# Optimization experiments

Hardware: AMD Instinct MI355X
Metric: run time of the kernel (lower is better)

## Reference

```python
import jax, jax.numpy as jnp
import numpy as np

EPS = 1e-6
H = 8          # num_heads
GAMMA = 0.99   # fixed decay (requires_grad=False in source)
RPE_LAYERS = 3


def srms(x):
    # SimpleRMSNorm: x / (rms(x) + eps), rms = ||x||_2 / sqrt(d) = sqrt(mean(x^2))
    return x / (jnp.sqrt(jnp.mean(x * x, axis=-1, keepdims=True)) + EPS)


def setup_inputs() -> dict:
    key = jax.random.key(0)
    B, N, E = 8, 2048, 512
    D1 = 1536            # int(3*512) // 8 * 8
    R = 512              # rpe_embedding
    ks = jax.random.split(key, 12)

    def lin(k, i, o):
        return jax.random.normal(k, (i, o), jnp.float32) * (i ** -0.5)

    x = jax.random.normal(ks[0], (B, N, E), jnp.float32)
    return {
        "x": x,
        "Wu": lin(ks[1], E, D1), "bu": jnp.zeros((D1,), jnp.float32),
        "Wv": lin(ks[2], E, D1), "bv": jnp.zeros((D1,), jnp.float32),
        "Wo": lin(ks[3], D1, E), "bo": jnp.zeros((E,), jnp.float32),
        "rpe_Win": lin(ks[4], 1, R), "rpe_bin": jnp.zeros((R,), jnp.float32),
        "rpe_W": jax.random.normal(ks[5], (RPE_LAYERS, R, R), jnp.float32) * (R ** -0.5),
        "rpe_b": jnp.zeros((RPE_LAYERS, R), jnp.float32),
        "rpe_Wout": lin(ks[6], R, D1), "rpe_bout": jnp.zeros((D1,), jnp.float32),
    }


def reference(x, Wu, bu, Wv, bv, Wo, bo, rpe_Win, rpe_bin, rpe_W, rpe_b, rpe_Wout, rpe_bout):
    B, N, E = x.shape
    u = jax.nn.silu(x @ Wu + bu)                     # b n d1
    v = jax.nn.silu(x @ Wv + bv)                     # b n d1
    D1 = v.shape[-1]
    D = D1 // H
    v = v.reshape(B, N, H, D).transpose(0, 2, 1, 3)  # b h n d

    # RPE MLP over positions: row 0 is the zero index, rows 1..N-1 are pos indices 1..N-1 (par_type=1)
    idx = jnp.arange(0, N, dtype=x.dtype)[:, None]   # (N, 1)
    h = idx @ rpe_Win + rpe_bin                      # (N, R)
    for i in range(RPE_LAYERS):                      # residual=False
        h = jax.nn.relu(srms(h)) @ rpe_W[i] + rpe_b[i]
    coeffs = jax.nn.relu(srms(h)) @ rpe_Wout + rpe_bout   # (N, H*D)
    coeffs = coeffs.reshape(N, H, D).transpose(1, 0, 2)   # h n d

    zero = coeffs[:, :1]                             # h 1 d  (a_0)
    pos = coeffs[:, 1:]                              # h n-1 d (a_1..a_{n-1})
    decay = GAMMA ** jnp.arange(1, N, dtype=x.dtype)[None, :, None]
    pos = pos * decay
    # causal: a = [a0, a1..a_{n-1}, a0]; act_type='none' -> identity
    a = jnp.concatenate([zero, pos, zero], axis=1)   # h, n+1, d

    # Toeplitz mixing via circular convolution of length 2n (torch.fft.rfft/irfft, norm='backward')
    m = 2 * N
    yf = jnp.fft.rfft(v, m, axis=2)                  # b h m/2+1 d (complex)
    af = jnp.fft.rfft(a, m, axis=1)[None]            # 1 h m/2+1 d
    out = jnp.fft.irfft(yf * af, m, axis=2)[:, :, :N, :]  # b h n d

    out = out.transpose(0, 2, 1, 3).reshape(B, N, D1)     # b n (h d)
    out = u * out
    return out @ Wo + bo
```

## Files before the change

### kernel.cpp

```cpp
#include <hip/hip_runtime.h>
#include <cstdint>


typedef unsigned short ushort_t;
typedef __attribute__((ext_vector_type(8))) short short8;
typedef __attribute__((ext_vector_type(4))) float f32x4;

#define AS1 __attribute__((address_space(1)))
#define AS3 __attribute__((address_space(3)))

#define SWZ(j) ((j) ^ (((j) >> 4) & 14))

__device__ __forceinline__ float bf2f(ushort_t b) {
  union { unsigned u; float f; } x; x.u = ((unsigned)b) << 16; return x.f;
}
__device__ __forceinline__ ushort_t f2bf(float f) {
  union { float f; unsigned u; } x; x.f = f;
  unsigned r = x.u + 0x7fffu + ((x.u >> 16) & 1u);
  return (ushort_t)(r >> 16);
}

__device__ __forceinline__ void gload_lds16(const void* g, void* l) {
  auto gp = reinterpret_cast<const AS1 unsigned*>(reinterpret_cast<uintptr_t>(g));
  auto lp = reinterpret_cast<AS3 unsigned*>(reinterpret_cast<uintptr_t>(l));
  __builtin_amdgcn_global_load_lds(gp, lp, 16, 0, 0);
}

template<int MODE>
__launch_bounds__(256, 2)
__global__ void gemm_bt(const ushort_t* __restrict__ A, const ushort_t* __restrict__ Bt,
                        const float* __restrict__ bias, void* __restrict__ Cout,
                        void* __restrict__ Cout2, int M, int N, int K, float lng)
{
  __shared__ ushort_t As[128 * 64];
  __shared__ ushort_t Bs[128 * 64];
  const int tid  = threadIdx.x;
  const int wave = tid >> 6, lane = tid & 63;
  const int nb = N >> 7;
  const int bm = (int)blockIdx.x / nb, bn = (int)blockIdx.x % nb;
  const int m0 = bm << 7, n0 = bn << 7;
  const int lrow = lane & 15, quad = lane >> 4;
  const int wm = (wave >> 1) << 6, wn = (wave & 1) << 6;
  const int srow = lane >> 3;
  const int scol = (lane & 7) << 3;

  f32x4 acc[4][4] = {};

  for (int kt = 0; kt < K; kt += 64) {
    __syncthreads();
#pragma unroll
    for (int i = 0; i < 4; ++i) {
      const int ci  = i * 4 + wave;
      const int row = ci * 8 + srow;
      gload_lds16(A  + (long)(m0 + row) * K + kt + scol, (void*)&As[ci * 512]);
      gload_lds16(Bt + (long)(n0 + row) * K + kt + scol, (void*)&Bs[ci * 512]);
    }
    __syncthreads();
#pragma unroll
    for (int s = 0; s < 2; ++s) {
      short8 afr[4], bfr[4];
#pragma unroll
      for (int i = 0; i < 4; ++i)
        afr[i] = *(const short8*)&As[(wm + i * 16 + lrow) * 64 + s * 32 + quad * 8];
#pragma unroll
      for (int j = 0; j < 4; ++j)
        bfr[j] = *(const short8*)&Bs[(wn + j * 16 + lrow) * 64 + s * 32 + quad * 8];
#pragma unroll
      for (int i = 0; i < 4; ++i)
#pragma unroll
        for (int j = 0; j < 4; ++j)
          acc[i][j] = __builtin_amdgcn_mfma_f32_16x16x32_bf16(afr[i], bfr[j], acc[i][j], 0, 0, 0);
    }
  }

#pragma unroll
  for (int i = 0; i < 4; ++i) {
    const int rowb = m0 + wm + i * 16 + quad * 4;
#pragma unroll
    for (int j = 0; j < 4; ++j) {
      const int col = n0 + wn + j * 16 + lrow;
      const float bv = bias[col];
      if (MODE == 0) {
#pragma unroll
        for (int r = 0; r < 4; ++r)
          ((float*)Cout)[(long)(rowb + r) * N + col] = acc[i][j][r] + bv;
      } else if (MODE == 2) {
#pragma unroll
        for (int r = 0; r < 4; ++r) {
          const int row = rowb + r;
          float dec = __expf(lng * (float)row);
          ((float*)Cout)[(long)col * M + row] = (acc[i][j][r] + bv) * dec;
        }
      } else {
        if (col < 1536) {
#pragma unroll
          for (int r = 0; r < 4; ++r) {
            float val = acc[i][j][r] + bv;
            float sv = val / (1.f + __expf(-val));
            ((ushort_t*)Cout)[(long)(rowb + r) * 1536 + col] = f2bf(sv);
          }
        } else {
          union { ushort_t h[4]; uint2 u2; } pk;
#pragma unroll
          for (int r = 0; r < 4; ++r) {
            float val = acc[i][j][r] + bv;
            float sv = val / (1.f + __expf(-val));
            pk.h[r] = f2bf(sv);
          }
          *(uint2*)((ushort_t*)Cout2 + (long)(col - 1536) * 16384 + rowb) = pk.u2;
        }
      }
    }
  }
}

__device__ __forceinline__ void srms_relu_store(float v0, float v1, ushort_t* out,
                                                long rowbase, int tid)
{
  float ss = v0 * v0 + v1 * v1;
#pragma unroll
  for (int off = 32; off; off >>= 1) ss += __shfl_down(ss, off);
  __shared__ float ps[4];
  const int wave = tid >> 6, lane = tid & 63;
  if (lane == 0) ps[wave] = ss;
  __syncthreads();
  float tot = ps[0] + ps[1] + ps[2] + ps[3];
  float sc = 1.f / (sqrtf(tot * (1.f / 512.f)) + 1e-6f);
  out[rowbase + tid]       = f2bf(fmaxf(v0 * sc, 0.f));
  out[rowbase + tid + 256] = f2bf(fmaxf(v1 * sc, 0.f));
}

__launch_bounds__(256)
__global__ void rpe_norm(const float* __restrict__ h, ushort_t* __restrict__ out)
{
  const int n = blockIdx.x, tid = threadIdx.x;
  float v0 = h[(long)n * 512 + tid];
  float v1 = h[(long)n * 512 + tid + 256];
  srms_relu_store(v0, v1, out, (long)n * 512, tid);
}

__device__ __forceinline__ void wtrans_body(const float* __restrict__ src,
                                            ushort_t* __restrict__ dst,
                                            int K, int N, int lb, int tid,
                                            float (*tile)[33])
{
  const int nbx = N >> 5;
  const int bx = lb % nbx, by = lb / nbx;
  const int n0 = bx << 5, k0 = by << 5;
  const int tx = tid & 31, ty = tid >> 5;
  for (int yy = ty; yy < 32; yy += 8)
    tile[yy][tx] = src[(long)(k0 + yy) * N + n0 + tx];
  __syncthreads();
  for (int yy = ty; yy < 32; yy += 8)
    dst[(long)(n0 + yy) * K + k0 + tx] = f2bf(tile[tx][yy]);
}

__launch_bounds__(256)
__global__ void prep_all(const float* __restrict__ Wu, const float* __restrict__ Wv,
                         const float* __restrict__ Wo, const float* __restrict__ rW,
                         const float* __restrict__ rWout,
                         const float* __restrict__ bu, const float* __restrict__ bv,
                         const float* __restrict__ x,
                         const float* __restrict__ rWin, const float* __restrict__ rbin,
                         ushort_t* __restrict__ wuvt, ushort_t* __restrict__ wot,
                         ushort_t* __restrict__ wrt, ushort_t* __restrict__ wroutt,
                         float* __restrict__ buvb, ushort_t* __restrict__ xb,
                         float2* __restrict__ twg, float2* __restrict__ twh,
                         ushort_t* __restrict__ a0)
{
  __shared__ float tile[32][33];
  const int bid = blockIdx.x, tid = threadIdx.x;
  if (bid < 3840) {
    const float* src; ushort_t* dst; int K, N, lb;
    if (bid < 768)       { src = Wu;    dst = wuvt;              K = 512;  N = 1536; lb = bid; }
    else if (bid < 1536) { src = Wv;    dst = wuvt + 1536L*512;  K = 512;  N = 1536; lb = bid - 768; }
    else if (bid < 2304) { src = Wo;    dst = wot;               K = 1536; N = 512;  lb = bid - 1536; }
    else if (bid < 2560) { src = rW;              dst = wrt;              K = 512; N = 512; lb = bid - 2304; }
    else if (bid < 2816) { src = rW + 512L*512;   dst = wrt + 512L*512;   K = 512; N = 512; lb = bid - 2560; }
    else if (bid < 3072) { src = rW + 2L*512*512; dst = wrt + 2L*512*512; K = 512; N = 512; lb = bid - 2816; }
    else                 { src = rWout; dst = wroutt;            K = 512;  N = 1536; lb = bid - 3072; }
    wtrans_body(src, dst, K, N, lb, tid, tile);
  } else if (bid < 3846) {
    int i = (bid - 3840) * 256 + tid;
    if (i < 1536) { buvb[i] = bu[i]; buvb[1536 + i] = bv[i]; }
  } else if (bid < 12038) {
    long i = (long)(bid - 3846) * 1024 + tid * 4;
    float4 f = *(const float4*)(x + i);
    unsigned lo = (unsigned)f2bf(f.x) | ((unsigned)f2bf(f.y) << 16);
    unsigned hi = (unsigned)f2bf(f.z) | ((unsigned)f2bf(f.w) << 16);
    *(uint2*)(xb + i) = make_uint2(lo, hi);
  } else if (bid < 12046) {
    int j = (bid - 12038) * 256 + tid;
    float s, c;
    __sincosf((float)j * (6.283185307179586f / 2048.f), &s, &c);
    twg[j] = make_float2(c, -s);
    if (j <= 1024) {
      float s2, c2;
      __sincosf((float)j * (3.14159265358979f / 2048.f), &s2, &c2);
      twh[j] = make_float2(c2, -s2);
    }
  } else {
    const int n = bid - 12046;
    const float fn = (float)n;
    float v0 = fn * rWin[tid] + rbin[tid];
    float v1 = fn * rWin[tid + 256] + rbin[tid + 256];
    srms_relu_store(v0, v1, a0, (long)n * 512, tid);
  }
}

__device__ __forceinline__ float2 cmulf(float2 a, float2 b) {
  return make_float2(a.x * b.x - a.y * b.y, a.x * b.y + a.y * b.x);
}

__device__ void fft2048_lds(float2* bx, float2* by, const float2* __restrict__ tw, int tid)
{
#pragma unroll
  for (int ii = 0; ii < 4; ++ii) {
    const int i = tid + ii * 256;
    float2 a = bx[SWZ(i)], b = bx[SWZ(i + 1024)];
    const int s = SWZ(2 * i);
    by[s]     = make_float2(a.x + b.x, a.y + b.y);
    by[s + 1] = make_float2(a.x - b.x, a.y - b.y);
  }
  __syncthreads();
  float2* src = by; float2* dst = bx;
#pragma unroll
  for (int ps = 0; ps < 5; ++ps) {
    const int p = 2 << (2 * ps);
    const int ts = 512 / p;
#pragma unroll
    for (int ii = 0; ii < 2; ++ii) {
      const int i = tid + ii * 256;
      const int k = i & (p - 1);
      float2 u0 = src[SWZ(i)],        u1 = src[SWZ(i + 512)];
      float2 u2 = src[SWZ(i + 1024)], u3 = src[SWZ(i + 1536)];
      const int tb = k * ts;
      float2 w1 = tw[tb], w2 = tw[2 * tb], w3 = tw[3 * tb];
      u1 = cmulf(u1, w1); u2 = cmulf(u2, w2); u3 = cmulf(u3, w3);
      float2 v0 = make_float2(u0.x + u2.x, u0.y + u2.y);
      float2 v2 = make_float2(u0.x - u2.x, u0.y - u2.y);
      float2 v1 = make_float2(u1.x + u3.x, u1.y + u3.y);
      float2 v3 = make_float2(u1.y - u3.y, u3.x - u1.x);
      const int j = ((i - k) << 2) + k;
      dst[SWZ(j)]         = make_float2(v0.x + v1.x, v0.y + v1.y);
      dst[SWZ(j + p)]     = make_float2(v2.x + v3.x, v2.y + v3.y);
      dst[SWZ(j + 2*p)]   = make_float2(v0.x - v1.x, v0.y - v1.y);
      dst[SWZ(j + 3*p)]   = make_float2(v2.x - v3.x, v2.y - v3.y);
    }
    __syncthreads();
    float2* t = src; src = dst; dst = t;
  }
}

__launch_bounds__(256)
__global__ void fft_kernel_spec(const float* __restrict__ kern, float2* __restrict__ af,
                                const float2* __restrict__ twg, const float2* __restrict__ twh)
{
  __shared__ float2 bx[2048], by[2048];
  const int tid = threadIdx.x, c = blockIdx.x;
  const float* kc = kern + (long)c * 2048;
  for (int j = tid; j < 1024; j += 256) bx[SWZ(j)] = *(const float2*)(kc + 2 * j);
  for (int j = tid + 1024; j < 2048; j += 256) bx[SWZ(j)] = make_float2(0.f, 0.f);
  __syncthreads();
  fft2048_lds(bx, by, twg, tid);
  float2* afc = af + (long)c * 2052;
  for (int k = tid; k <= 1024; k += 256) {
    float2 Zk = bx[SWZ(k)], Zn = bx[SWZ((2048 - k) & 2047)];
    float2 E = make_float2(0.5f * (Zk.x + Zn.x), 0.5f * (Zk.y - Zn.y));
    float2 O = make_float2(0.5f * (Zk.y + Zn.y), 0.5f * (Zn.x - Zk.x));
    float2 W = twh[k];
    float2 WO = cmulf(W, O);
    afc[k] = make_float2(E.x + WO.x, E.y + WO.y);
    if (k != 0 && k != 1024)
      afc[2048 - k] = make_float2(E.x - WO.x, -(E.y - WO.y));
    if (k == 0)
      afc[2048] = make_float2(E.x - WO.x, -(E.y - WO.y));
  }
}

__launch_bounds__(256)
__global__ void fft_conv(ushort_t* __restrict__ vt, const float2* __restrict__ af,
                         const float2* __restrict__ twg, const float2* __restrict__ twh)
{
  __shared__ float2 bx[2048], by[2048];
  const int tid = threadIdx.x;
  const int c = (int)blockIdx.x >> 3;
  ushort_t* vs = vt + (long)blockIdx.x * 2048;
  for (int j = tid; j < 1024; j += 256) {
    unsigned pv = *(const unsigned*)(vs + 2 * j);
    bx[SWZ(j)] = make_float2(bf2f((ushort_t)(pv & 0xffffu)), bf2f((ushort_t)(pv >> 16)));
  }
  for (int j = tid + 1024; j < 2048; j += 256) bx[SWZ(j)] = make_float2(0.f, 0.f);
  __syncthreads();
  fft2048_lds(bx, by, twg, tid);
  const float2* afc = af + (long)c * 2052;
  for (int k = tid; k <= 1024; k += 256) {
    float2 Zk = bx[SWZ(k)], Zn = bx[SWZ((2048 - k) & 2047)];
    float2 E = make_float2(0.5f * (Zk.x + Zn.x), 0.5f * (Zk.y - Zn.y));
    float2 O = make_float2(0.5f * (Zk.y + Zn.y), 0.5f * (Zn.x - Zk.x));
    float2 W = twh[k];
    float2 WO = cmulf(W, O);
    float2 Xk = make_float2(E.x + WO.x, E.y + WO.y);
    float2 Xn = make_float2(E.x - WO.x, -(E.y - WO.y));
    float2 Pk = cmulf(Xk, afc[k]);
    float2 Pn = cmulf(Xn, afc[2048 - k]);
    float2 E2 = make_float2(0.5f * (Pk.x + Pn.x), 0.5f * (Pk.y - Pn.y));
    float2 G  = make_float2(0.5f * (Pk.x - Pn.x), 0.5f * (Pk.y + Pn.y));
    float2 cW = make_float2(W.x, -W.y);
    float2 Fo = cmulf(cW, G);
    by[SWZ(k)] = make_float2(E2.x - Fo.y, -(E2.y + Fo.x));
    if (k != 0 && k != 1024) {
      const int kn = 2048 - k;
      by[SWZ(kn)] = make_float2(E2.x + Fo.y, E2.y - Fo.x);
    }
  }
  __syncthreads();
  fft2048_lds(by, bx, twg, tid);
  const float inv = 1.f / 2048.f;
  for (int j = tid; j < 1024; j += 256) {
    float2 r = by[SWZ(j)];
    unsigned ov = (unsigned)f2bf(r.x * inv) | ((unsigned)f2bf(-r.y * inv) << 16);
    *(unsigned*)(vs + 2 * j) = ov;
  }
}

__launch_bounds__(256)
__global__ void gate_trans(const ushort_t* __restrict__ convt, ushort_t* __restrict__ u)
{
  __shared__ ushort_t tile[64][65];
  const int bc = (int)blockIdx.x % 24, br = (int)blockIdx.x / 24;
  const int c0 = bc << 6, r0 = br << 6;
  const int tx = threadIdx.x & 63, ty = threadIdx.x >> 6;
  for (int yy = ty; yy < 64; yy += 4)
    tile[yy][tx] = convt[(long)(c0 + yy) * 16384 + r0 + tx];
  __syncthreads();
  for (int yy = ty; yy < 64; yy += 4) {
    long ui = (long)(r0 + yy) * 1536 + c0 + tx;
    float uu = bf2f(u[ui]);
    float cc = bf2f(tile[tx][yy]);
    u[ui] = f2bf(uu * cc);
  }
}

extern "C" void kernel_launch(void* const* d_in, const int* in_sizes, int n_in,
                              void* d_out, int out_size, void* d_ws, size_t ws_size,
                              hipStream_t stream)
{
  const float* x     = (const float*)d_in[0];
  const float* Wu    = (const float*)d_in[1];
  const float* bu    = (const float*)d_in[2];
  const float* Wv    = (const float*)d_in[3];
  const float* bv    = (const float*)d_in[4];
  const float* Wo    = (const float*)d_in[5];
  const float* bo    = (const float*)d_in[6];
  const float* rWin  = (const float*)d_in[7];
  const float* rbin  = (const float*)d_in[8];
  const float* rW    = (const float*)d_in[9];
  const float* rb    = (const float*)d_in[10];
  const float* rWout = (const float*)d_in[11];
  const float* rbout = (const float*)d_in[12];

  char* base = (char*)d_ws;
  size_t off = 0;
  auto alloc = [&](size_t bytes) -> char* {
    size_t r = (off + 255) & ~(size_t)255; off = r + bytes; return base + r;
  };
  ushort_t* wuvt   = (ushort_t*)alloc(3072L * 512 * 2);
  ushort_t* wot    = (ushort_t*)alloc(512L * 1536 * 2);
  ushort_t* wrt    = (ushort_t*)alloc(3L * 512 * 512 * 2);
  ushort_t* wroutt = (ushort_t*)alloc(1536L * 512 * 2);
  float*    buvb   = (float*)   alloc(3072L * 4);
  ushort_t* a0     = (ushort_t*)alloc(2048L * 512 * 2);
  float2*   af     = (float2*)  alloc(1536L * 2052 * 8);
  float2*   twg    = (float2*)  alloc(2048L * 8);
  float2*   twh    = (float2*)  alloc(1025L * 8);
  char*     X      = alloc(16384L * 512 * 2);
  ushort_t* u      = (ushort_t*)alloc(16384L * 1536 * 2);
  ushort_t* vt     = (ushort_t*)alloc(1536L * 16384 * 2);
  ushort_t* xb   = (ushort_t*)X;
  float*    h    = (float*)X;
  float*    kern = (float*)(X + 4L * 1024 * 1024);

  const float lng = -0.01005033585350145f;

  prep_all<<<dim3(14094), dim3(256), 0, stream>>>(
      Wu, Wv, Wo, rW, rWout, bu, bv, x, rWin, rbin,
      wuvt, wot, wrt, wroutt, buvb, xb, twg, twh, a0);

  gemm_bt<3><<<dim3(3072), dim3(256), 0, stream>>>(xb, wuvt, buvb, u, vt,
                                                   16384, 3072, 512, 0.f);

  for (int i = 0; i < 3; ++i) {
    gemm_bt<0><<<dim3(64), dim3(256), 0, stream>>>(a0, wrt + (long)i * 512 * 512,
                                                   rb + (long)i * 512, h, nullptr,
                                                   2048, 512, 512, 0.f);
    rpe_norm<<<dim3(2048), dim3(256), 0, stream>>>(h, a0);
  }
  gemm_bt<2><<<dim3(192), dim3(256), 0, stream>>>(a0, wroutt, rbout, kern, nullptr,
                                                  2048, 1536, 512, lng);
  fft_kernel_spec<<<dim3(1536), dim3(256), 0, stream>>>(kern, af, twg, twh);

  fft_conv<<<dim3(12288), dim3(256), 0, stream>>>(vt, af, twg, twh);
  gate_trans<<<dim3(6144), dim3(256), 0, stream>>>(vt, u);
  gemm_bt<0><<<dim3(512), dim3(256), 0, stream>>>(u, wot, bo, d_out, nullptr,
                                                  16384, 512, 1536, 0.f);
}
```

Baseline: 530.8 us.

## Replace radix-2/4 LDS FFT with radix-8 stages and half-zero first pass

```diff
diff --git a/kernel.cpp b/kernel.cpp
--- a/kernel.cpp
+++ b/kernel.cpp
@@ -9,7 +9,8 @@
 #define AS1 __attribute__((address_space(1)))
 #define AS3 __attribute__((address_space(3)))
 
-#define SWZ(j) ((j) ^ (((j) >> 4) & 14))
+#define SW1(j) ((j) ^ (((j) >> 4) & 15))
+#define SW2(j) ((j) ^ ((((j) >> 6) & 7) << 1))
 
 __device__ __forceinline__ float bf2f(ushort_t b) {
   union { unsigned u; float f; } x; x.u = ((unsigned)b) << 16; return x.f;
@@ -211,45 +212,87 @@
 __device__ __forceinline__ float2 cmulf(float2 a, float2 b) {
   return make_float2(a.x * b.x - a.y * b.y, a.x * b.y + a.y * b.x);
 }
-
-__device__ void fft2048_lds(float2* bx, float2* by, const float2* __restrict__ tw, int tid)
-{
-#pragma unroll
-  for (int ii = 0; ii < 4; ++ii) {
-    const int i = tid + ii * 256;
-    float2 a = bx[SWZ(i)], b = bx[SWZ(i + 1024)];
-    const int s = SWZ(2 * i);
-    by[s]     = make_float2(a.x + b.x, a.y + b.y);
-    by[s + 1] = make_float2(a.x - b.x, a.y - b.y);
-  }
-  __syncthreads();
-  float2* src = by; float2* dst = bx;
-#pragma unroll
-  for (int ps = 0; ps < 5; ++ps) {
-    const int p = 2 << (2 * ps);
-    const int ts = 512 / p;
-#pragma unroll
-    for (int ii = 0; ii < 2; ++ii) {
-      const int i = tid + ii * 256;
-      const int k = i & (p - 1);
-      float2 u0 = src[SWZ(i)],        u1 = src[SWZ(i + 512)];
-      float2 u2 = src[SWZ(i + 1024)], u3 = src[SWZ(i + 1536)];
-      const int tb = k * ts;
-      float2 w1 = tw[tb], w2 = tw[2 * tb], w3 = tw[3 * tb];
-      u1 = cmulf(u1, w1); u2 = cmulf(u2, w2); u3 = cmulf(u3, w3);
-      float2 v0 = make_float2(u0.x + u2.x, u0.y + u2.y);
-      float2 v2 = make_float2(u0.x - u2.x, u0.y - u2.y);
-      float2 v1 = make_float2(u1.x + u3.x, u1.y + u3.y);
-      float2 v3 = make_float2(u1.y - u3.y, u3.x - u1.x);
-      const int j = ((i - k) << 2) + k;
-      dst[SWZ(j)]         = make_float2(v0.x + v1.x, v0.y + v1.y);
-      dst[SWZ(j + p)]     = make_float2(v2.x + v3.x, v2.y + v3.y);
-      dst[SWZ(j + 2*p)]   = make_float2(v0.x - v1.x, v0.y - v1.y);
-      dst[SWZ(j + 3*p)]   = make_float2(v2.x - v3.x, v2.y - v3.y);
-    }
-    __syncthreads();
-    float2* t = src; src = dst; dst = t;
-  }
+__device__ __forceinline__ float2 cadd(float2 a, float2 b){ return make_float2(a.x+b.x, a.y+b.y); }
+__device__ __forceinline__ float2 csub(float2 a, float2 b){ return make_float2(a.x-b.x, a.y-b.y); }
+__device__ __forceinline__ float2 cmni(float2 z){ return make_float2(z.y, -z.x); }
+__device__ __forceinline__ float2 cw8(float2 z){
+  const float s = 0.70710678118654752f;
+  return make_float2(s*(z.x+z.y), s*(z.y-z.x));
+}
+__device__ __forceinline__ float2 cw83(float2 z){
+  const float s = 0.70710678118654752f;
+  return make_float2(s*(z.y-z.x), -s*(z.x+z.y));
+}
+
+__device__ __forceinline__ void dft8(const float2* u, float2* y)
+{
+  float2 a0=cadd(u[0],u[4]), a1=cadd(u[1],u[5]), a2=cadd(u[2],u[6]), a3=cadd(u[3],u[7]);
+  float2 b0=csub(u[0],u[4]), b1=cw8(csub(u[1],u[5])), b2=cmni(csub(u[2],u[6])), b3=cw83(csub(u[3],u[7]));
+  float2 c0=cadd(a0,a2), c1=csub(a0,a2), c2=cadd(a1,a3), c3=cmni(csub(a1,a3));
+  y[0]=cadd(c0,c2); y[2]=cadd(c1,c3); y[4]=csub(c0,c2); y[6]=csub(c1,c3);
+  float2 d0=cadd(b0,b2), d1=csub(b0,b2), d2=cadd(b1,b3), d3=cmni(csub(b1,b3));
+  y[1]=cadd(d0,d2); y[3]=cadd(d1,d3); y[5]=csub(d0,d2); y[7]=csub(d1,d3);
+}
+__device__ __forceinline__ void dft8_hz(const float2* u, float2* y)
+{
+  float2 b1=cw8(u[1]), b2=cmni(u[2]), b3=cw83(u[3]);
+  float2 c0=cadd(u[0],u[2]), c1=csub(u[0],u[2]), c2=cadd(u[1],u[3]), c3=cmni(csub(u[1],u[3]));
+  y[0]=cadd(c0,c2); y[2]=cadd(c1,c3); y[4]=csub(c0,c2); y[6]=csub(c1,c3);
+  float2 d0=cadd(u[0],b2), d1=csub(u[0],b2), d2=cadd(b1,b3), d3=cmni(csub(b1,b3));
+  y[1]=cadd(d0,d2); y[3]=cadd(d1,d3); y[5]=csub(d0,d2); y[7]=csub(d1,d3);
+}
+
+template<bool HZ>
+__device__ void fft2048_r8(float2* b0, float2* b1, const float2* __restrict__ tw, int tid)
+{
+  float2 u[8], y[8];
+  {
+    const int i = tid;
+#pragma unroll
+    for (int m = 0; m < (HZ ? 4 : 8); ++m) u[m] = b0[i + 256 * m];
+    if (HZ) dft8_hz(u, y); else dft8(u, y);
+    const int j = i << 3;
+#pragma unroll
+    for (int m = 0; m < 8; ++m) b1[SW1(j + m)] = y[m];
+  }
+  __syncthreads();
+  {
+    const int i = tid, k = i & 7, tb = k << 5;
+#pragma unroll
+    for (int m = 0; m < 8; ++m) u[m] = b1[SW1(i + 256 * m)];
+#pragma unroll
+    for (int m = 1; m < 8; ++m) u[m] = cmulf(u[m], tw[m * tb]);
+    dft8(u, y);
+    const int j = ((i - k) << 3) + k;
+#pragma unroll
+    for (int m = 0; m < 8; ++m) b0[SW2(j + (m << 3))] = y[m];
+  }
+  __syncthreads();
+  {
+    const int i = tid, k = i & 63, tb = k << 2;
+#pragma unroll
+    for (int m = 0; m < 8; ++m) u[m] = b0[SW2(i + 256 * m)];
+#pragma unroll
+    for (int m = 1; m < 8; ++m) u[m] = cmulf(u[m], tw[m * tb]);
+    dft8(u, y);
+    const int j = ((i - k) << 3) + k;
+#pragma unroll
+    for (int m = 0; m < 8; ++m) b1[j + (m << 6)] = y[m];
+  }
+  __syncthreads();
+#pragma unroll
+  for (int h = 0; h < 2; ++h) {
+    const int i = tid + (h << 8);
+    float2 q0 = b1[i], q1 = b1[i + 512], q2 = b1[i + 1024], q3 = b1[i + 1536];
+    q1 = cmulf(q1, tw[i]); q2 = cmulf(q2, tw[2 * i]); q3 = cmulf(q3, tw[3 * i]);
+    float2 v0 = cadd(q0, q2), v2 = csub(q0, q2);
+    float2 v1 = cadd(q1, q3), v3 = cmni(csub(q1, q3));
+    b0[i]        = cadd(v0, v1);
+    b0[i + 512]  = cadd(v2, v3);
+    b0[i + 1024] = csub(v0, v1);
+    b0[i + 1536] = csub(v2, v3);
+  }
+  __syncthreads();
 }
 
 __launch_bounds__(256)
@@ -259,13 +302,12 @@
   __shared__ float2 bx[2048], by[2048];
   const int tid = threadIdx.x, c = blockIdx.x;
   const float* kc = kern + (long)c * 2048;
-  for (int j = tid; j < 1024; j += 256) bx[SWZ(j)] = *(const float2*)(kc + 2 * j);
-  for (int j = tid + 1024; j < 2048; j += 256) bx[SWZ(j)] = make_float2(0.f, 0.f);
-  __syncthreads();
-  fft2048_lds(bx, by, twg, tid);
+  for (int j = tid; j < 1024; j += 256) bx[j] = *(const float2*)(kc + 2 * j);
+  __syncthreads();
+  fft2048_r8<true>(bx, by, twg, tid);
   float2* afc = af + (long)c * 2052;
   for (int k = tid; k <= 1024; k += 256) {
-    float2 Zk = bx[SWZ(k)], Zn = bx[SWZ((2048 - k) & 2047)];
+    float2 Zk = bx[k], Zn = bx[(2048 - k) & 2047];
     float2 E = make_float2(0.5f * (Zk.x + Zn.x), 0.5f * (Zk.y - Zn.y));
     float2 O = make_float2(0.5f * (Zk.y + Zn.y), 0.5f * (Zn.x - Zk.x));
     float2 W = twh[k];
@@ -286,16 +328,17 @@
   const int tid = threadIdx.x;
   const int c = (int)blockIdx.x >> 3;
   ushort_t* vs = vt + (long)blockIdx.x * 2048;
-  for (int j = tid; j < 1024; j += 256) {
+#pragma unroll
+  for (int jj = 0; jj < 4; ++jj) {
+    const int j = tid + jj * 256;
     unsigned pv = *(const unsigned*)(vs + 2 * j);
-    bx[SWZ(j)] = make_float2(bf2f((ushort_t)(pv & 0xffffu)), bf2f((ushort_t)(pv >> 16)));
-  }
-  for (int j = tid + 1024; j < 2048; j += 256) bx[SWZ(j)] = make_float2(0.f, 0.f);
-  __syncthreads();
-  fft2048_lds(bx, by, twg, tid);
+    bx[j] = make_float2(bf2f((ushort_t)(pv & 0xffffu)), bf2f((ushort_t)(pv >> 16)));
+  }
+  __syncthreads();
+  fft2048_r8<true>(bx, by, twg, tid);
   const float2* afc = af + (long)c * 2052;
   for (int k = tid; k <= 1024; k += 256) {
-    float2 Zk = bx[SWZ(k)], Zn = bx[SWZ((2048 - k) & 2047)];
+    float2 Zk = bx[k], Zn = bx[(2048 - k) & 2047];
     float2 E = make_float2(0.5f * (Zk.x + Zn.x), 0.5f * (Zk.y - Zn.y));
     float2 O = make_float2(0.5f * (Zk.y + Zn.y), 0.5f * (Zn.x - Zk.x));
     float2 W = twh[k];
@@ -308,17 +351,19 @@
     float2 G  = make_float2(0.5f * (Pk.x - Pn.x), 0.5f * (Pk.y + Pn.y));
     float2 cW = make_float2(W.x, -W.y);
     float2 Fo = cmulf(cW, G);
-    by[SWZ(k)] = make_float2(E2.x - Fo.y, -(E2.y + Fo.x));
+    by[k] = make_float2(E2.x - Fo.y, -(E2.y + Fo.x));
     if (k != 0 && k != 1024) {
       const int kn = 2048 - k;
-      by[SWZ(kn)] = make_float2(E2.x + Fo.y, E2.y - Fo.x);
+      by[kn] = make_float2(E2.x + Fo.y, E2.y - Fo.x);
     }
   }
   __syncthreads();
-  fft2048_lds(by, bx, twg, tid);
+  fft2048_r8<false>(by, bx, twg, tid);
   const float inv = 1.f / 2048.f;
-  for (int j = tid; j < 1024; j += 256) {
-    float2 r = by[SWZ(j)];
+#pragma unroll
+  for (int jj = 0; jj < 4; ++jj) {
+    const int j = tid + jj * 256;
+    float2 r = by[j];
     unsigned ov = (unsigned)f2bf(r.x * inv) | ((unsigned)f2bf(-r.y * inv) << 16);
     *(unsigned*)(vs + 2 * j) = ov;
   }
```

New measurement: 511.0 us. 3.7% less time.
